# Kernel tuning notes

Hardware: AMD Instinct MI355X
Metric: run time of the kernel (lower is better)

Reference implementation:

```python
import jax, jax.numpy as jnp
import numpy as np
from jax import lax

H = 2048          # hidden_size
I = 1408          # moe_intermediate_size
E = 16            # n_routed_experts
K = 4             # num_experts_per_tok
N_SHARED = 2      # n_shared_experts
IS = I * N_SHARED # shared expert intermediate
B, S = 1, 1024


def setup_inputs() -> dict:
    key = jax.random.key(0)
    ks = jax.random.split(key, 8)
    scale = 0.02
    return {
        "hidden_states": jax.random.normal(ks[0], (B, S, H), dtype=jnp.float32),
        "gate_w": jax.random.normal(ks[1], (E, H), dtype=jnp.float32) * scale,  # MoEGate.weight
        "w_gate": jax.random.normal(ks[2], (E, H, I), dtype=jnp.float32) * scale,
        "w_up": jax.random.normal(ks[3], (E, H, I), dtype=jnp.float32) * scale,
        "w_down": jax.random.normal(ks[4], (E, I, H), dtype=jnp.float32) * scale,
        "sw_gate": jax.random.normal(ks[5], (H, IS), dtype=jnp.float32) * scale,
        "sw_up": jax.random.normal(ks[6], (H, IS), dtype=jnp.float32) * scale,
        "sw_down": jax.random.normal(ks[7], (IS, H), dtype=jnp.float32) * scale,
    }


def _moe_forward(hidden_states, gate_w, w_gate, w_up, w_down, sw_gate, sw_up, sw_down):
    bsz, seq_len, h = hidden_states.shape
    flat = hidden_states.reshape(-1, h)                # [T, H]
    T = flat.shape[0]

    # --- MoEGate: softmax scoring + top-k (norm_topk_prob=False) ---
    logits = flat @ gate_w.T                           # [T, E]
    scores = jax.nn.softmax(logits, axis=-1)
    topk_w, topk_idx = lax.top_k(scores, K)            # [T, K]

    # combine[t, e] = sum of top-k weights assigned to expert e (scatter of dispatch)
    combine = jnp.zeros((T, E), dtype=flat.dtype).at[
        jnp.arange(T)[:, None], topk_idx
    ].add(topk_w)                                      # [T, E]

    # --- routed experts: scan over experts, accumulate weighted SwiGLU MLP outputs ---
    def step(y, xs):
        wg, wu, wd, c = xs                             # [H,I], [H,I], [I,H], [T]
        out = (jax.nn.silu(flat @ wg) * (flat @ wu)) @ wd   # [T, H]
        return y + c[:, None] * out, None

    y, _ = lax.scan(step, jnp.zeros_like(flat), (w_gate, w_up, w_down, combine.T))

    # --- shared experts (always-on SwiGLU MLP with larger intermediate) ---
    shared = (jax.nn.silu(flat @ sw_gate) * (flat @ sw_up)) @ sw_down  # [T, H]

    return (y + shared).reshape(bsz, seq_len, h)


def reference(hidden_states, gate_w, w_gate, w_up, w_down, sw_gate, sw_up, sw_down):
    return _moe_forward(hidden_states, gate_w, w_gate, w_up, w_down,
                        sw_gate, sw_up, sw_down)
```

## Files before the change

### kernel.cpp

```cpp
#include <hip/hip_runtime.h>
#include <hip/hip_bf16.h>
#include <stdint.h>

#define T_TOK 1024
#define H_DIM 2048
#define I_DIM 1408
#define E_NUM 16
#define K_TOP 4
#define IS_DIM 2816
#define BK 64
#define BKP 72
#define BM 256
#define NT_MAX 40

typedef __hip_bfloat16 bf;
typedef __attribute__((ext_vector_type(8))) __bf16 bf16x8;
typedef __attribute__((ext_vector_type(4))) float f32x4;

__device__ __forceinline__ void gload16(const void* g, void* l) {
  __builtin_amdgcn_global_load_lds((const __attribute__((address_space(1))) void*)g,
                                   (__attribute__((address_space(3))) void*)l, 16, 0, 0);
}

__global__ void cvt_x_kernel(const float* __restrict__ in, bf* __restrict__ out) {
  int i = blockIdx.x * blockDim.x + threadIdx.x;
  float4 v = reinterpret_cast<const float4*>(in)[i];
  int b = i * 4;
  out[b + 0] = __float2bfloat16(v.x);
  out[b + 1] = __float2bfloat16(v.y);
  out[b + 2] = __float2bfloat16(v.z);
  out[b + 3] = __float2bfloat16(v.w);
}

__global__ void gate_topk_kernel(const float* __restrict__ x, const float* __restrict__ gw,
                                 int* __restrict__ topk_idx, float* __restrict__ topk_w) {
  int t = blockIdx.x;
  int lane = threadIdx.x;
  float acc[E_NUM];
#pragma unroll
  for (int e = 0; e < E_NUM; e++) acc[e] = 0.f;
  const float* xt = x + (long)t * H_DIM;
  for (int h = lane; h < H_DIM; h += 64) {
    float xv = xt[h];
#pragma unroll
    for (int e = 0; e < E_NUM; e++) acc[e] += xv * gw[e * H_DIM + h];
  }
#pragma unroll
  for (int e = 0; e < E_NUM; e++) {
    float v = acc[e];
    for (int off = 32; off; off >>= 1) v += __shfl_xor(v, off, 64);
    acc[e] = v;
  }
  if (lane == 0) {
    float m = acc[0];
#pragma unroll
    for (int e = 1; e < E_NUM; e++) m = fmaxf(m, acc[e]);
    float sc[E_NUM];
    float s = 0.f;
#pragma unroll
    for (int e = 0; e < E_NUM; e++) { sc[e] = expf(acc[e] - m); s += sc[e]; }
    float inv = 1.f / s;
#pragma unroll
    for (int e = 0; e < E_NUM; e++) sc[e] *= inv;
    for (int k = 0; k < K_TOP; k++) {
      int bi = 0;
      float bv = sc[0];
      for (int e = 1; e < E_NUM; e++)
        if (sc[e] > bv) { bv = sc[e]; bi = e; }
      topk_idx[t * K_TOP + k] = bi;
      topk_w[t * K_TOP + k] = bv;
      sc[bi] = -1.f;
    }
  }
}

__global__ void build_lists_kernel(const int* __restrict__ topk_idx,
                                   int* __restrict__ rows, int* __restrict__ tile_expert,
                                   int* __restrict__ n_tiles) {
  __shared__ int cnt[E_NUM], cur[E_NUM], s_tb;
  int tid = threadIdx.x;
  if (tid < E_NUM) cnt[tid] = 0;
  __syncthreads();
  for (int p = tid; p < T_TOK * K_TOP; p += blockDim.x)
    atomicAdd(&cnt[topk_idx[p]], 1);
  __syncthreads();
  if (tid == 0) {
    int tb = 0;
    for (int e = 0; e < E_NUM; e++) {
      int nt = (cnt[e] + BM - 1) / BM;
      cur[e] = tb * BM;
      for (int j = 0; j < nt; j++) tile_expert[tb + j] = e;
      tb += nt;
    }
    for (int j = 0; j < 8; j++) tile_expert[tb + j] = 16 + (j >> 2);
    s_tb = tb;
    *n_tiles = tb + 8;
  }
  __syncthreads();
  int tb = s_tb;
  for (int r = tid; r < NT_MAX * BM; r += blockDim.x) rows[r] = -1;
  __syncthreads();
  for (int p = tid; p < T_TOK * K_TOP; p += blockDim.x) {
    int t = p >> 2, k = p & 3;
    int e = topk_idx[p];
    int slot = atomicAdd(&cur[e], 1);
    rows[slot] = t * 8 + k;
  }
  for (int idx = tid; idx < 8 * BM; idx += blockDim.x) {
    int j = idx >> 8, r = idx & 255;
    int t = (j & 3) * BM + r;
    rows[(tb + j) * BM + r] = t * 8 + 4 + (j >> 2);
  }
}

__launch_bounds__(512, 4)
__global__ void gemm_gateup_kernel(const bf* __restrict__ xb,
                                   const int* __restrict__ rows,
                                   const int* __restrict__ tile_expert,
                                   const int* __restrict__ n_tiles,
                                   const float* __restrict__ Wg,
                                   const float* __restrict__ Wu,
                                   const float* __restrict__ SWg,
                                   const float* __restrict__ SWu,
                                   bf* __restrict__ act) {
  int bid = blockIdx.x;
  int idx = (bid & 7) * 110 + (bid >> 3);
  int x = idx / NT_MAX, rt = idx % NT_MAX;
  if (rt >= *n_tiles) return;
  int e = tile_expert[rt];
  bool sh = e >= 16;
  const float* gbase = sh ? (SWg + (e - 16) * I_DIM) : (Wg + (long)e * H_DIM * I_DIM);
  const float* ubase = sh ? (SWu + (e - 16) * I_DIM) : (Wu + (long)e * H_DIM * I_DIM);
  long bstride = sh ? IS_DIM : I_DIM;
  int i0 = x * 64;

  __shared__ bf lA[BM * BK];
  __shared__ bf lB2[2][64 * BKP];

  int tid = threadIdx.x, w = tid >> 6, lane = tid & 63;
  int l15 = lane & 15, lhi = lane >> 4;
  int nq = tid & 15, mt = (tid >> 4) & 1, kq = (tid >> 5) & 7, jh = tid >> 8;
  int sswz = (((lane & 7) ^ (lane >> 3)) * 8);
  int bco = (kq ^ (nq & 7)) * 8 + jh * 4;

  const bf* asrc[4];
#pragma unroll
  for (int i = 0; i < 4; i++) {
    int rr = rt * BM + i * 64 + w * 8 + (lane >> 3);
    int p = rows[rr];
    int tok = (p >= 0) ? (p >> 3) : 0;
    asrc[i] = xb + (long)tok * H_DIM + sswz;
  }

  const float* psrc = (mt ? ubase : gbase) + i0 + nq * 4 + (long)(kq * 8 + jh * 4) * bstride;

  f32x4 accg[4][2], accu[4][2];
  f32x4 z4 = {0.f, 0.f, 0.f, 0.f};
#pragma unroll
  for (int m = 0; m < 4; m++)
#pragma unroll
    for (int n = 0; n < 2; n++) { accg[m][n] = z4; accu[m][n] = z4; }

  int wr = w >> 1, wc = w & 1;
  for (int kt = 0; kt < H_DIM; kt += BK) {
    float4 v[4];
    const float* p_ = psrc + (long)kt * bstride;
#pragma unroll
    for (int j = 0; j < 4; j++)
      v[j] = *reinterpret_cast<const float4*>(p_ + (long)j * bstride);
    __syncthreads();
#pragma unroll
    for (int i = 0; i < 4; i++)
      gload16(asrc[i] + kt, lA + (i * 64 + w * 8) * BK);
#pragma unroll
    for (int c = 0; c < 4; c++) {
      union { short4 s4; bf b[4]; } o;
#pragma unroll
      for (int j = 0; j < 4; j++)
        o.b[j] = __float2bfloat16(((const float*)&v[j])[c]);
      *reinterpret_cast<short4*>(&lB2[mt][(nq * 4 + c) * BKP + bco]) = o.s4;
    }
    __syncthreads();
#pragma unroll
    for (int kk = 0; kk < 2; kk++) {
      bf16x8 af[4];
#pragma unroll
      for (int m = 0; m < 4; m++)
        af[m] = *reinterpret_cast<const bf16x8*>(
            lA + (wr * 64 + m * 16 + l15) * BK + (((kk * 4 + lhi) ^ (l15 & 7)) * 8));
#pragma unroll
      for (int n = 0; n < 2; n++) {
        int nrow = wc * 32 + n * 16 + l15;
        int bch = ((kk * 4 + lhi) ^ ((nrow >> 2) & 7)) * 8;
        bf16x8 gf = *reinterpret_cast<const bf16x8*>(&lB2[0][nrow * BKP + bch]);
        bf16x8 uf = *reinterpret_cast<const bf16x8*>(&lB2[1][nrow * BKP + bch]);
#pragma unroll
        for (int m = 0; m < 4; m++) {
          accg[m][n] = __builtin_amdgcn_mfma_f32_16x16x32_bf16(af[m], gf, accg[m][n], 0, 0, 0);
          accu[m][n] = __builtin_amdgcn_mfma_f32_16x16x32_bf16(af[m], uf, accu[m][n], 0, 0, 0);
        }
      }
    }
  }

#pragma unroll
  for (int m = 0; m < 4; m++)
#pragma unroll
    for (int n = 0; n < 2; n++)
#pragma unroll
      for (int r2 = 0; r2 < 4; r2++) {
        float gv = accg[m][n][r2];
        float uv = accu[m][n][r2];
        float s = (gv / (1.f + __expf(-gv))) * uv;
        int row = rt * BM + wr * 64 + m * 16 + lhi * 4 + r2;
        int col = i0 + wc * 32 + n * 16 + l15;
        act[(long)row * I_DIM + col] = __float2bfloat16(s);
      }
}

__launch_bounds__(512, 4)
__global__ void gemm_down_kernel(const bf* __restrict__ A,
                                 const int* __restrict__ rows,
                                 const int* __restrict__ tile_expert,
                                 const int* __restrict__ n_tiles,
                                 const float* __restrict__ Wd,
                                 const float* __restrict__ SWd,
                                 bf* __restrict__ outp) {
  int bid = blockIdx.x;
  int idx = (bid & 7) * 80 + (bid >> 3);
  int x = idx / NT_MAX, rt = idx % NT_MAX;
  if (rt >= *n_tiles) return;
  int e = tile_expert[rt];
  bool sh = e >= 16;
  const float* bbase = sh ? (SWd + (long)(e - 16) * I_DIM * H_DIM)
                          : (Wd + (long)e * I_DIM * H_DIM);
  int h0 = x * 128;

  __shared__ bf lA[BM * BK];
  __shared__ bf lB[128 * BKP];
  __shared__ int rowsl[BM];

  int tid = threadIdx.x, w = tid >> 6, lane = tid & 63;
  int l15 = lane & 15, lhi = lane >> 4;
  int ng = tid & 31, kq = (tid >> 5) & 7, jh = tid >> 8;
  int sswz = (((lane & 7) ^ (lane >> 3)) * 8);
  int bco = (kq ^ (ng & 7)) * 8 + jh * 4;
  if (tid < BM) rowsl[tid] = rows[rt * BM + tid];

  const bf* asrc[4];
#pragma unroll
  for (int i = 0; i < 4; i++)
    asrc[i] = A + (long)(rt * BM + i * 64 + w * 8 + (lane >> 3)) * I_DIM + sswz;

  const float* psrc = bbase + h0 + ng * 4 + (long)(kq * 8 + jh * 4) * H_DIM;

  f32x4 acc[4][4];
  f32x4 z4 = {0.f, 0.f, 0.f, 0.f};
#pragma unroll
  for (int m = 0; m < 4; m++)
#pragma unroll
    for (int n = 0; n < 4; n++) acc[m][n] = z4;

  int wr = w >> 1, wc = w & 1;
  for (int kt = 0; kt < I_DIM; kt += BK) {
    float4 v[4];
    const float* p_ = psrc + (long)kt * H_DIM;
#pragma unroll
    for (int j = 0; j < 4; j++)
      v[j] = *reinterpret_cast<const float4*>(p_ + (long)j * H_DIM);
    __syncthreads();
#pragma unroll
    for (int i = 0; i < 4; i++)
      gload16(asrc[i] + kt, lA + (i * 64 + w * 8) * BK);
#pragma unroll
    for (int c = 0; c < 4; c++) {
      union { short4 s4; bf b[4]; } o;
#pragma unroll
      for (int j = 0; j < 4; j++)
        o.b[j] = __float2bfloat16(((const float*)&v[j])[c]);
      *reinterpret_cast<short4*>(&lB[(ng * 4 + c) * BKP + bco]) = o.s4;
    }
    __syncthreads();
#pragma unroll
    for (int kk = 0; kk < 2; kk++) {
      bf16x8 af[4];
#pragma unroll
      for (int m = 0; m < 4; m++)
        af[m] = *reinterpret_cast<const bf16x8*>(
            lA + (wr * 64 + m * 16 + l15) * BK + (((kk * 4 + lhi) ^ (l15 & 7)) * 8));
#pragma unroll
      for (int n = 0; n < 4; n++) {
        int nrow = wc * 64 + n * 16 + l15;
        int bch = ((kk * 4 + lhi) ^ ((nrow >> 2) & 7)) * 8;
        bf16x8 bfr = *reinterpret_cast<const bf16x8*>(&lB[nrow * BKP + bch]);
#pragma unroll
        for (int m = 0; m < 4; m++)
          acc[m][n] = __builtin_amdgcn_mfma_f32_16x16x32_bf16(af[m], bfr, acc[m][n], 0, 0, 0);
      }
    }
  }

#pragma unroll
  for (int m = 0; m < 4; m++)
#pragma unroll
    for (int n = 0; n < 4; n++)
#pragma unroll
      for (int r2 = 0; r2 < 4; r2++) {
        int lrow = wr * 64 + m * 16 + lhi * 4 + r2;
        int col = h0 + wc * 64 + n * 16 + l15;
        int p = rowsl[lrow];
        if (p >= 0) outp[(long)p * H_DIM + col] = __float2bfloat16(acc[m][n][r2]);
      }
}

__global__ void combine_kernel(const bf* __restrict__ outp,
                               const float* __restrict__ topk_w,
                               float* __restrict__ out) {
  int g = blockIdx.x * blockDim.x + threadIdx.x;
  int t = g >> 8;
  int h = (g & 255) * 8;
  const bf* base = outp + (long)t * 8 * H_DIM + h;
  float w0 = topk_w[t * 4 + 0], w1 = topk_w[t * 4 + 1];
  float w2 = topk_w[t * 4 + 2], w3 = topk_w[t * 4 + 3];
  bf16x8 s4 = *reinterpret_cast<const bf16x8*>(base + 4 * H_DIM);
  bf16x8 s5 = *reinterpret_cast<const bf16x8*>(base + 5 * H_DIM);
  bf16x8 r0 = *reinterpret_cast<const bf16x8*>(base + 0 * H_DIM);
  bf16x8 r1 = *reinterpret_cast<const bf16x8*>(base + 1 * H_DIM);
  bf16x8 r2 = *reinterpret_cast<const bf16x8*>(base + 2 * H_DIM);
  bf16x8 r3 = *reinterpret_cast<const bf16x8*>(base + 3 * H_DIM);
  float acc[8];
#pragma unroll
  for (int j = 0; j < 8; j++) {
    acc[j] = (float)s4[j] + (float)s5[j]
           + w0 * (float)r0[j] + w1 * (float)r1[j]
           + w2 * (float)r2[j] + w3 * (float)r3[j];
  }
  float4* o = reinterpret_cast<float4*>(out + (long)t * H_DIM + h);
  o[0] = make_float4(acc[0], acc[1], acc[2], acc[3]);
  o[1] = make_float4(acc[4], acc[5], acc[6], acc[7]);
}

extern "C" void kernel_launch(void* const* d_in, const int* in_sizes, int n_in,
                              void* d_out, int out_size, void* d_ws, size_t ws_size,
                              hipStream_t stream) {
  const float* x     = (const float*)d_in[0];
  const float* gw    = (const float*)d_in[1];
  const float* wgate = (const float*)d_in[2];
  const float* wup   = (const float*)d_in[3];
  const float* wdown = (const float*)d_in[4];
  const float* swg   = (const float*)d_in[5];
  const float* swu   = (const float*)d_in[6];
  const float* swd   = (const float*)d_in[7];
  float* out = (float*)d_out;

  char* ws = (char*)d_ws;
  size_t off = 0;
  auto alloc = [&](size_t bytes) {
    void* p = ws + off;
    off += (bytes + 255) & ~(size_t)255;
    return p;
  };

  bf* xb   = (bf*)alloc((size_t)T_TOK * H_DIM * 2);
  bf* act  = (bf*)alloc((size_t)NT_MAX * BM * I_DIM * 2);
  bf* outp = (bf*)alloc((size_t)T_TOK * 8 * H_DIM * 2);
  int*   topk_idx = (int*)alloc(T_TOK * K_TOP * 4);
  float* topk_w   = (float*)alloc(T_TOK * K_TOP * 4);
  int*   rowsbuf  = (int*)alloc(NT_MAX * BM * 4);
  int*   tile_exp = (int*)alloc(NT_MAX * 4);
  int*   n_tiles  = (int*)alloc(64);
  (void)ws_size; (void)in_sizes; (void)n_in; (void)out_size;

  hipLaunchKernelGGL(cvt_x_kernel, dim3(T_TOK * H_DIM / 1024), dim3(256), 0, stream, x, xb);
  hipLaunchKernelGGL(gate_topk_kernel, dim3(T_TOK), dim3(64), 0, stream, x, gw, topk_idx, topk_w);
  hipLaunchKernelGGL(build_lists_kernel, dim3(1), dim3(256), 0, stream, topk_idx, rowsbuf, tile_exp, n_tiles);

  hipLaunchKernelGGL(gemm_gateup_kernel, dim3(22 * NT_MAX), dim3(512), 0, stream,
                     xb, rowsbuf, tile_exp, n_tiles, wgate, wup, swg, swu, act);
  hipLaunchKernelGGL(gemm_down_kernel, dim3(16 * NT_MAX), dim3(512), 0, stream,
                     act, rowsbuf, tile_exp, n_tiles, wdown, swd, outp);

  hipLaunchKernelGGL(combine_kernel, dim3(T_TOK * H_DIM / 8 / 256), dim3(256), 0, stream,
                     outp, topk_w, out);
}
```

Before: 321.9 us.

## Double-buffer GEMM K-loop with async fp32 weight staging through LDS

New measurement: 472.9 us. 1.47x slower.

```diff
diff --git a/kernel.cpp b/kernel.cpp
--- a/kernel.cpp
+++ b/kernel.cpp
@@ -113,7 +113,7 @@
   }
 }
 
-__launch_bounds__(512, 4)
+__launch_bounds__(512, 2)
 __global__ void gemm_gateup_kernel(const bf* __restrict__ xb,
                                    const int* __restrict__ rows,
                                    const int* __restrict__ tile_expert,
@@ -134,14 +134,13 @@
   long bstride = sh ? IS_DIM : I_DIM;
   int i0 = x * 64;
 
-  __shared__ bf lA[BM * BK];
+  __shared__ bf lA[2][BM * BK];
+  __shared__ float stg[2][2][64 * 64];
   __shared__ bf lB2[2][64 * BKP];
 
   int tid = threadIdx.x, w = tid >> 6, lane = tid & 63;
   int l15 = lane & 15, lhi = lane >> 4;
-  int nq = tid & 15, mt = (tid >> 4) & 1, kq = (tid >> 5) & 7, jh = tid >> 8;
   int sswz = (((lane & 7) ^ (lane >> 3)) * 8);
-  int bco = (kq ^ (nq & 7)) * 8 + jh * 4;
 
   const bf* asrc[4];
 #pragma unroll
@@ -152,7 +151,12 @@
     asrc[i] = xb + (long)tok * H_DIM + sswz;
   }
 
-  const float* psrc = (mt ? ubase : gbase) + i0 + nq * 4 + (long)(kq * 8 + jh * 4) * bstride;
+  int bwm = w >> 2;
+  const float* bmat = bwm ? ubase : gbase;
+  const float* bsrc = bmat + i0 + (lane & 15) * 4 + (long)((w & 3) * 16 + (lane >> 4)) * bstride;
+  int brow = (w & 3) * 16;
+
+  int cnq = tid & 15, ckh = (tid >> 4) & 1, ckg = (tid >> 5) & 7, cmt = tid >> 8;
 
   f32x4 accg[4][2], accu[4][2];
   f32x4 z4 = {0.f, 0.f, 0.f, 0.f};
@@ -162,46 +166,69 @@
     for (int n = 0; n < 2; n++) { accg[m][n] = z4; accu[m][n] = z4; }
 
   int wr = w >> 1, wc = w & 1;
-  for (int kt = 0; kt < H_DIM; kt += BK) {
-    float4 v[4];
-    const float* p_ = psrc + (long)kt * bstride;
-#pragma unroll
-    for (int j = 0; j < 4; j++)
-      v[j] = *reinterpret_cast<const float4*>(p_ + (long)j * bstride);
-    __syncthreads();
-#pragma unroll
-    for (int i = 0; i < 4; i++)
-      gload16(asrc[i] + kt, lA + (i * 64 + w * 8) * BK);
-#pragma unroll
-    for (int c = 0; c < 4; c++) {
-      union { short4 s4; bf b[4]; } o;
-#pragma unroll
-      for (int j = 0; j < 4; j++)
-        o.b[j] = __float2bfloat16(((const float*)&v[j])[c]);
-      *reinterpret_cast<short4*>(&lB2[mt][(nq * 4 + c) * BKP + bco]) = o.s4;
-    }
-    __syncthreads();
-#pragma unroll
-    for (int kk = 0; kk < 2; kk++) {
-      bf16x8 af[4];
-#pragma unroll
-      for (int m = 0; m < 4; m++)
-        af[m] = *reinterpret_cast<const bf16x8*>(
-            lA + (wr * 64 + m * 16 + l15) * BK + (((kk * 4 + lhi) ^ (l15 & 7)) * 8));
-#pragma unroll
-      for (int n = 0; n < 2; n++) {
-        int nrow = wc * 32 + n * 16 + l15;
-        int bch = ((kk * 4 + lhi) ^ ((nrow >> 2) & 7)) * 8;
-        bf16x8 gf = *reinterpret_cast<const bf16x8*>(&lB2[0][nrow * BKP + bch]);
-        bf16x8 uf = *reinterpret_cast<const bf16x8*>(&lB2[1][nrow * BKP + bch]);
-#pragma unroll
-        for (int m = 0; m < 4; m++) {
-          accg[m][n] = __builtin_amdgcn_mfma_f32_16x16x32_bf16(af[m], gf, accg[m][n], 0, 0, 0);
-          accu[m][n] = __builtin_amdgcn_mfma_f32_16x16x32_bf16(af[m], uf, accu[m][n], 0, 0, 0);
-        }
-      }
-    }
-  }
+
+#define GU_ISSUE(T, NB)                                                              \
+  {                                                                                  \
+    _Pragma("unroll") for (int i = 0; i < 4; i++)                                    \
+        gload16(asrc[i] + (T) * BK, &lA[NB][(i * 64 + w * 8) * BK]);                 \
+    const float* bs_ = bsrc + (long)(T) * BK * bstride;                              \
+    _Pragma("unroll") for (int q = 0; q < 4; q++)                                    \
+        gload16(bs_ + (long)(q * 4) * bstride, &stg[NB][bwm][(brow + q * 4) * 64]);  \
+  }
+
+#define GU_CONVERT(CB)                                                               \
+  {                                                                                  \
+    float4 cv[4];                                                                    \
+    _Pragma("unroll") for (int j = 0; j < 4; j++)                                    \
+        cv[j] = *reinterpret_cast<const float4*>(                                    \
+            &stg[CB][cmt][(ckg * 8 + ckh * 4 + j) * 64 + cnq * 4]);                  \
+    _Pragma("unroll") for (int c = 0; c < 4; c++) {                                  \
+      union { short4 s4; bf b[4]; } o;                                               \
+      _Pragma("unroll") for (int j = 0; j < 4; j++)                                  \
+          o.b[j] = __float2bfloat16(((const float*)&cv[j])[c]);                      \
+      *reinterpret_cast<short4*>(                                                    \
+          &lB2[cmt][(cnq * 4 + c) * BKP + (ckg ^ (cnq & 7)) * 8 + ckh * 4]) = o.s4;  \
+    }                                                                                \
+  }
+
+#define GU_MFMA(CB)                                                                  \
+  {                                                                                  \
+    _Pragma("unroll") for (int kk = 0; kk < 2; kk++) {                               \
+      bf16x8 af[4];                                                                  \
+      _Pragma("unroll") for (int m = 0; m < 4; m++)                                  \
+          af[m] = *reinterpret_cast<const bf16x8*>(                                  \
+              &lA[CB][(wr * 64 + m * 16 + l15) * BK + (((kk * 4 + lhi) ^ (l15 & 7)) * 8)]); \
+      _Pragma("unroll") for (int n = 0; n < 2; n++) {                                \
+        int nrow = wc * 32 + n * 16 + l15;                                           \
+        int bch = ((kk * 4 + lhi) ^ ((nrow >> 2) & 7)) * 8;                          \
+        bf16x8 gf = *reinterpret_cast<const bf16x8*>(&lB2[0][nrow * BKP + bch]);     \
+        bf16x8 uf = *reinterpret_cast<const bf16x8*>(&lB2[1][nrow * BKP + bch]);     \
+        _Pragma("unroll") for (int m = 0; m < 4; m++) {                              \
+          accg[m][n] = __builtin_amdgcn_mfma_f32_16x16x32_bf16(af[m], gf, accg[m][n], 0, 0, 0); \
+          accu[m][n] = __builtin_amdgcn_mfma_f32_16x16x32_bf16(af[m], uf, accu[m][n], 0, 0, 0); \
+        }                                                                            \
+      }                                                                              \
+    }                                                                                \
+  }
+
+  const int NT = H_DIM / BK;
+  GU_ISSUE(0, 0);
+
+  for (int t = 0; t < NT; ++t) {
+    int cur = t & 1, nxt = cur ^ 1;
+    asm volatile("s_waitcnt vmcnt(0)" ::: "memory");
+    __builtin_amdgcn_s_barrier();
+    __builtin_amdgcn_sched_barrier(0);
+    if (t + 1 < NT) GU_ISSUE(t + 1, nxt);
+    GU_CONVERT(cur);
+    asm volatile("s_waitcnt lgkmcnt(0)" ::: "memory");
+    __builtin_amdgcn_s_barrier();
+    __builtin_amdgcn_sched_barrier(0);
+    GU_MFMA(cur);
+  }
+#undef GU_ISSUE
+#undef GU_CONVERT
+#undef GU_MFMA
 
 #pragma unroll
   for (int m = 0; m < 4; m++)
@@ -218,7 +245,7 @@
       }
 }
 
-__launch_bounds__(512, 4)
+__launch_bounds__(512, 2)
 __global__ void gemm_down_kernel(const bf* __restrict__ A,
                                  const int* __restrict__ rows,
                                  const int* __restrict__ tile_expert,
@@ -236,15 +263,14 @@
                           : (Wd + (long)e * I_DIM * H_DIM);
   int h0 = x * 128;
 
-  __shared__ bf lA[BM * BK];
+  __shared__ bf lA[2][BM * BK];
+  __shared__ float stg[2][64 * 128];
   __shared__ bf lB[128 * BKP];
   __shared__ int rowsl[BM];
 
   int tid = threadIdx.x, w = tid >> 6, lane = tid & 63;
   int l15 = lane & 15, lhi = lane >> 4;
-  int ng = tid & 31, kq = (tid >> 5) & 7, jh = tid >> 8;
   int sswz = (((lane & 7) ^ (lane >> 3)) * 8);
-  int bco = (kq ^ (ng & 7)) * 8 + jh * 4;
   if (tid < BM) rowsl[tid] = rows[rt * BM + tid];
 
   const bf* asrc[4];
@@ -252,7 +278,10 @@
   for (int i = 0; i < 4; i++)
     asrc[i] = A + (long)(rt * BM + i * 64 + w * 8 + (lane >> 3)) * I_DIM + sswz;
 
-  const float* psrc = bbase + h0 + ng * 4 + (long)(kq * 8 + jh * 4) * H_DIM;
+  const float* bsrc = bbase + h0 + (lane & 31) * 4 + (long)(w * 8 + (lane >> 5)) * H_DIM;
+  int brow = w * 8;
+
+  int cng = tid & 31, ckg = (tid >> 5) & 7, cch = tid >> 8;
 
   f32x4 acc[4][4];
   f32x4 z4 = {0.f, 0.f, 0.f, 0.f};
@@ -262,43 +291,66 @@
     for (int n = 0; n < 4; n++) acc[m][n] = z4;
 
   int wr = w >> 1, wc = w & 1;
-  for (int kt = 0; kt < I_DIM; kt += BK) {
-    float4 v[4];
-    const float* p_ = psrc + (long)kt * H_DIM;
-#pragma unroll
-    for (int j = 0; j < 4; j++)
-      v[j] = *reinterpret_cast<const float4*>(p_ + (long)j * H_DIM);
-    __syncthreads();
-#pragma unroll
-    for (int i = 0; i < 4; i++)
-      gload16(asrc[i] + kt, lA + (i * 64 + w * 8) * BK);
-#pragma unroll
-    for (int c = 0; c < 4; c++) {
-      union { short4 s4; bf b[4]; } o;
-#pragma unroll
-      for (int j = 0; j < 4; j++)
-        o.b[j] = __float2bfloat16(((const float*)&v[j])[c]);
-      *reinterpret_cast<short4*>(&lB[(ng * 4 + c) * BKP + bco]) = o.s4;
-    }
-    __syncthreads();
-#pragma unroll
-    for (int kk = 0; kk < 2; kk++) {
-      bf16x8 af[4];
-#pragma unroll
-      for (int m = 0; m < 4; m++)
-        af[m] = *reinterpret_cast<const bf16x8*>(
-            lA + (wr * 64 + m * 16 + l15) * BK + (((kk * 4 + lhi) ^ (l15 & 7)) * 8));
-#pragma unroll
-      for (int n = 0; n < 4; n++) {
-        int nrow = wc * 64 + n * 16 + l15;
-        int bch = ((kk * 4 + lhi) ^ ((nrow >> 2) & 7)) * 8;
-        bf16x8 bfr = *reinterpret_cast<const bf16x8*>(&lB[nrow * BKP + bch]);
-#pragma unroll
-        for (int m = 0; m < 4; m++)
-          acc[m][n] = __builtin_amdgcn_mfma_f32_16x16x32_bf16(af[m], bfr, acc[m][n], 0, 0, 0);
-      }
-    }
-  }
+
+#define DN_ISSUE(T, NB)                                                              \
+  {                                                                                  \
+    _Pragma("unroll") for (int i = 0; i < 4; i++)                                    \
+        gload16(asrc[i] + (T) * BK, &lA[NB][(i * 64 + w * 8) * BK]);                 \
+    const float* bs_ = bsrc + (long)(T) * BK * H_DIM;                                \
+    _Pragma("unroll") for (int q = 0; q < 4; q++)                                    \
+        gload16(bs_ + (long)(q * 2) * H_DIM, &stg[NB][(brow + q * 2) * 128]);        \
+  }
+
+#define DN_CONVERT(CB)                                                              \
+  {                                                                                 \
+    float2 cv[8];                                                                   \
+    _Pragma("unroll") for (int j = 0; j < 8; j++)                                   \
+        cv[j] = *reinterpret_cast<const float2*>(                                   \
+            &stg[CB][(ckg * 8 + j) * 128 + cng * 4 + cch * 2]);                     \
+    _Pragma("unroll") for (int c = 0; c < 2; c++) {                                 \
+      union { bf16x8 vv; bf b[8]; } o;                                              \
+      _Pragma("unroll") for (int j = 0; j < 8; j++)                                 \
+          o.b[j] = __float2bfloat16(((const float*)&cv[j])[c]);                     \
+      *reinterpret_cast<bf16x8*>(                                                   \
+          &lB[(cng * 4 + cch * 2 + c) * BKP + (ckg ^ (cng & 7)) * 8]) = o.vv;       \
+    }                                                                               \
+  }
+
+#define DN_MFMA(CB)                                                                 \
+  {                                                                                 \
+    _Pragma("unroll") for (int kk = 0; kk < 2; kk++) {                              \
+      bf16x8 af[4];                                                                 \
+      _Pragma("unroll") for (int m = 0; m < 4; m++)                                 \
+          af[m] = *reinterpret_cast<const bf16x8*>(                                 \
+              &lA[CB][(wr * 64 + m * 16 + l15) * BK + (((kk * 4 + lhi) ^ (l15 & 7)) * 8)]); \
+      _Pragma("unroll") for (int n = 0; n < 4; n++) {                               \
+        int nrow = wc * 64 + n * 16 + l15;                                          \
+        int bch = ((kk * 4 + lhi) ^ ((nrow >> 2) & 7)) * 8;                         \
+        bf16x8 bfr = *reinterpret_cast<const bf16x8*>(&lB[nrow * BKP + bch]);       \
+        _Pragma("unroll") for (int m = 0; m < 4; m++)                               \
+            acc[m][n] = __builtin_amdgcn_mfma_f32_16x16x32_bf16(af[m], bfr, acc[m][n], 0, 0, 0); \
+      }                                                                             \
+    }                                                                               \
+  }
+
+  const int NT = I_DIM / BK;
+  DN_ISSUE(0, 0);
+
+  for (int t = 0; t < NT; ++t) {
+    int cur = t & 1, nxt = cur ^ 1;
+    asm volatile("s_waitcnt vmcnt(0)" ::: "memory");
+    __builtin_amdgcn_s_barrier();
+    __builtin_amdgcn_sched_barrier(0);
+    if (t + 1 < NT) DN_ISSUE(t + 1, nxt);
+    DN_CONVERT(cur);
+    asm volatile("s_waitcnt lgkmcnt(0)" ::: "memory");
+    __builtin_amdgcn_s_barrier();
+    __builtin_amdgcn_sched_barrier(0);
+    DN_MFMA(cur);
+  }
+#undef DN_ISSUE
+#undef DN_CONVERT
+#undef DN_MFMA
 
 #pragma unroll
   for (int m = 0; m < 4; m++)
```

## Retile MoE GEMMs to 384-row tiles with narrower N and 6 waves

Applied to the files above, without the earlier changes.

After: 459.7 us. +42.8%, slower.

```diff
diff --git a/kernel.cpp b/kernel.cpp
--- a/kernel.cpp
+++ b/kernel.cpp
@@ -10,8 +10,8 @@
 #define IS_DIM 2816
 #define BK 64
 #define BKP 72
-#define BM 256
-#define NT_MAX 40
+#define BM 384
+#define NT_MAX 32
 
 typedef __hip_bfloat16 bf;
 typedef __attribute__((ext_vector_type(8))) __bf16 bf16x8;
@@ -92,9 +92,9 @@
       for (int j = 0; j < nt; j++) tile_expert[tb + j] = e;
       tb += nt;
     }
-    for (int j = 0; j < 8; j++) tile_expert[tb + j] = 16 + (j >> 2);
+    for (int j = 0; j < 6; j++) tile_expert[tb + j] = 16 + (j / 3);
     s_tb = tb;
-    *n_tiles = tb + 8;
+    *n_tiles = tb + 6;
   }
   __syncthreads();
   int tb = s_tb;
@@ -106,14 +106,14 @@
     int slot = atomicAdd(&cur[e], 1);
     rows[slot] = t * 8 + k;
   }
-  for (int idx = tid; idx < 8 * BM; idx += blockDim.x) {
-    int j = idx >> 8, r = idx & 255;
-    int t = (j & 3) * BM + r;
-    rows[(tb + j) * BM + r] = t * 8 + 4 + (j >> 2);
-  }
-}
-
-__launch_bounds__(512, 4)
+  for (int idx = tid; idx < 6 * BM; idx += blockDim.x) {
+    int j = idx / BM, r = idx % BM;
+    int t = (j % 3) * BM + r;
+    if (t < T_TOK) rows[(tb + j) * BM + r] = t * 8 + 4 + (j / 3);
+  }
+}
+
+__launch_bounds__(384, 2)
 __global__ void gemm_gateup_kernel(const bf* __restrict__ xb,
                                    const int* __restrict__ rows,
                                    const int* __restrict__ tile_expert,
@@ -124,36 +124,37 @@
                                    const float* __restrict__ SWu,
                                    bf* __restrict__ act) {
   int bid = blockIdx.x;
-  int idx = (bid & 7) * 110 + (bid >> 3);
-  int x = idx / NT_MAX, rt = idx % NT_MAX;
+  int idx = (bid & 7) * 176 + (bid >> 3);
+  int x = idx >> 5, rt = idx & 31;
   if (rt >= *n_tiles) return;
   int e = tile_expert[rt];
   bool sh = e >= 16;
   const float* gbase = sh ? (SWg + (e - 16) * I_DIM) : (Wg + (long)e * H_DIM * I_DIM);
   const float* ubase = sh ? (SWu + (e - 16) * I_DIM) : (Wu + (long)e * H_DIM * I_DIM);
   long bstride = sh ? IS_DIM : I_DIM;
-  int i0 = x * 64;
+  int i0 = x * 32;
 
   __shared__ bf lA[BM * BK];
-  __shared__ bf lB2[2][64 * BKP];
+  __shared__ bf lB2[2][32 * BKP];
 
   int tid = threadIdx.x, w = tid >> 6, lane = tid & 63;
   int l15 = lane & 15, lhi = lane >> 4;
-  int nq = tid & 15, mt = (tid >> 4) & 1, kq = (tid >> 5) & 7, jh = tid >> 8;
   int sswz = (((lane & 7) ^ (lane >> 3)) * 8);
-  int bco = (kq ^ (nq & 7)) * 8 + jh * 4;
-
-  const bf* asrc[4];
-#pragma unroll
-  for (int i = 0; i < 4; i++) {
-    int rr = rt * BM + i * 64 + w * 8 + (lane >> 3);
+
+  bool stager = tid < 256;
+  int smat = tid >> 7, sr = tid & 127, nc = sr & 7, kq = sr >> 3;
+  const float* psrc = (smat ? ubase : gbase) + i0 + nc * 4 + (long)(kq * 4) * bstride;
+  int bslot = (((kq >> 1) ^ nc) * 16 + (kq & 1) * 8) / 2;
+
+  const bf* asrc[8];
+#pragma unroll
+  for (int i = 0; i < 8; i++) {
+    int rr = rt * BM + i * 48 + w * 8 + (lane >> 3);
     int p = rows[rr];
     int tok = (p >= 0) ? (p >> 3) : 0;
     asrc[i] = xb + (long)tok * H_DIM + sswz;
   }
 
-  const float* psrc = (mt ? ubase : gbase) + i0 + nq * 4 + (long)(kq * 8 + jh * 4) * bstride;
-
   f32x4 accg[4][2], accu[4][2];
   f32x4 z4 = {0.f, 0.f, 0.f, 0.f};
 #pragma unroll
@@ -161,24 +162,27 @@
 #pragma unroll
     for (int n = 0; n < 2; n++) { accg[m][n] = z4; accu[m][n] = z4; }
 
-  int wr = w >> 1, wc = w & 1;
   for (int kt = 0; kt < H_DIM; kt += BK) {
     float4 v[4];
-    const float* p_ = psrc + (long)kt * bstride;
-#pragma unroll
-    for (int j = 0; j < 4; j++)
-      v[j] = *reinterpret_cast<const float4*>(p_ + (long)j * bstride);
+    if (stager) {
+      const float* p_ = psrc + (long)kt * bstride;
+#pragma unroll
+      for (int j = 0; j < 4; j++)
+        v[j] = *reinterpret_cast<const float4*>(p_ + (long)j * bstride);
+    }
     __syncthreads();
 #pragma unroll
-    for (int i = 0; i < 4; i++)
-      gload16(asrc[i] + kt, lA + (i * 64 + w * 8) * BK);
-#pragma unroll
-    for (int c = 0; c < 4; c++) {
-      union { short4 s4; bf b[4]; } o;
-#pragma unroll
-      for (int j = 0; j < 4; j++)
-        o.b[j] = __float2bfloat16(((const float*)&v[j])[c]);
-      *reinterpret_cast<short4*>(&lB2[mt][(nq * 4 + c) * BKP + bco]) = o.s4;
+    for (int i = 0; i < 8; i++)
+      gload16(asrc[i] + kt, lA + (i * 48 + w * 8) * BK);
+    if (stager) {
+#pragma unroll
+      for (int c = 0; c < 4; c++) {
+        union { short4 s4; bf b[4]; } o;
+#pragma unroll
+        for (int j = 0; j < 4; j++)
+          o.b[j] = __float2bfloat16(((const float*)&v[j])[c]);
+        *reinterpret_cast<short4*>(&lB2[smat][(nc * 4 + c) * BKP + bslot]) = o.s4;
+      }
     }
     __syncthreads();
 #pragma unroll
@@ -187,10 +191,10 @@
 #pragma unroll
       for (int m = 0; m < 4; m++)
         af[m] = *reinterpret_cast<const bf16x8*>(
-            lA + (wr * 64 + m * 16 + l15) * BK + (((kk * 4 + lhi) ^ (l15 & 7)) * 8));
+            lA + (w * 64 + m * 16 + l15) * BK + (((kk * 4 + lhi) ^ (l15 & 7)) * 8));
 #pragma unroll
       for (int n = 0; n < 2; n++) {
-        int nrow = wc * 32 + n * 16 + l15;
+        int nrow = n * 16 + l15;
         int bch = ((kk * 4 + lhi) ^ ((nrow >> 2) & 7)) * 8;
         bf16x8 gf = *reinterpret_cast<const bf16x8*>(&lB2[0][nrow * BKP + bch]);
         bf16x8 uf = *reinterpret_cast<const bf16x8*>(&lB2[1][nrow * BKP + bch]);
@@ -212,13 +216,13 @@
         float gv = accg[m][n][r2];
         float uv = accu[m][n][r2];
         float s = (gv / (1.f + __expf(-gv))) * uv;
-        int row = rt * BM + wr * 64 + m * 16 + lhi * 4 + r2;
-        int col = i0 + wc * 32 + n * 16 + l15;
+        int row = rt * BM + w * 64 + m * 16 + lhi * 4 + r2;
+        int col = i0 + n * 16 + l15;
         act[(long)row * I_DIM + col] = __float2bfloat16(s);
       }
 }
 
-__launch_bounds__(512, 4)
+__launch_bounds__(384, 2)
 __global__ void gemm_down_kernel(const bf* __restrict__ A,
                                  const int* __restrict__ rows,
                                  const int* __restrict__ tile_expert,
@@ -227,32 +231,33 @@
                                  const float* __restrict__ SWd,
                                  bf* __restrict__ outp) {
   int bid = blockIdx.x;
-  int idx = (bid & 7) * 80 + (bid >> 3);
-  int x = idx / NT_MAX, rt = idx % NT_MAX;
+  int idx = (bid & 7) * 128 + (bid >> 3);
+  int x = idx >> 5, rt = idx & 31;
   if (rt >= *n_tiles) return;
   int e = tile_expert[rt];
   bool sh = e >= 16;
   const float* bbase = sh ? (SWd + (long)(e - 16) * I_DIM * H_DIM)
                           : (Wd + (long)e * I_DIM * H_DIM);
-  int h0 = x * 128;
+  int h0 = x * 64;
 
   __shared__ bf lA[BM * BK];
-  __shared__ bf lB[128 * BKP];
+  __shared__ bf lB[64 * BKP];
   __shared__ int rowsl[BM];
 
   int tid = threadIdx.x, w = tid >> 6, lane = tid & 63;
   int l15 = lane & 15, lhi = lane >> 4;
-  int ng = tid & 31, kq = (tid >> 5) & 7, jh = tid >> 8;
   int sswz = (((lane & 7) ^ (lane >> 3)) * 8);
-  int bco = (kq ^ (ng & 7)) * 8 + jh * 4;
-  if (tid < BM) rowsl[tid] = rows[rt * BM + tid];
-
-  const bf* asrc[4];
-#pragma unroll
-  for (int i = 0; i < 4; i++)
-    asrc[i] = A + (long)(rt * BM + i * 64 + w * 8 + (lane >> 3)) * I_DIM + sswz;
-
-  const float* psrc = bbase + h0 + ng * 4 + (long)(kq * 8 + jh * 4) * H_DIM;
+  for (int r = tid; r < BM; r += 384) rowsl[r] = rows[rt * BM + r];
+
+  bool stager = tid < 256;
+  int nc = tid & 15, kq = tid >> 4;
+  const float* psrc = bbase + h0 + nc * 4 + (long)(kq * 4) * H_DIM;
+  int bslot = (((kq >> 1) ^ (nc & 7)) * 16 + (kq & 1) * 8) / 2;
+
+  const bf* asrc[8];
+#pragma unroll
+  for (int i = 0; i < 8; i++)
+    asrc[i] = A + (long)(rt * BM + i * 48 + w * 8 + (lane >> 3)) * I_DIM + sswz;
 
   f32x4 acc[4][4];
   f32x4 z4 = {0.f, 0.f, 0.f, 0.f};
@@ -261,24 +266,27 @@
 #pragma unroll
     for (int n = 0; n < 4; n++) acc[m][n] = z4;
 
-  int wr = w >> 1, wc = w & 1;
   for (int kt = 0; kt < I_DIM; kt += BK) {
     float4 v[4];
-    const float* p_ = psrc + (long)kt * H_DIM;
-#pragma unroll
-    for (int j = 0; j < 4; j++)
-      v[j] = *reinterpret_cast<const float4*>(p_ + (long)j * H_DIM);
+    if (stager) {
+      const float* p_ = psrc + (long)kt * H_DIM;
+#pragma unroll
+      for (int j = 0; j < 4; j++)
+        v[j] = *reinterpret_cast<const float4*>(p_ + (long)j * H_DIM);
+    }
     __syncthreads();
 #pragma unroll
-    for (int i = 0; i < 4; i++)
-      gload16(asrc[i] + kt, lA + (i * 64 + w * 8) * BK);
-#pragma unroll
-    for (int c = 0; c < 4; c++) {
-      union { short4 s4; bf b[4]; } o;
-#pragma unroll
-      for (int j = 0; j < 4; j++)
-        o.b[j] = __float2bfloat16(((const float*)&v[j])[c]);
-      *reinterpret_cast<short4*>(&lB[(ng * 4 + c) * BKP + bco]) = o.s4;
+    for (int i = 0; i < 8; i++)
+      gload16(asrc[i] + kt, lA + (i * 48 + w * 8) * BK);
+    if (stager) {
+#pragma unroll
+      for (int c = 0; c < 4; c++) {
+        union { short4 s4; bf b[4]; } o;
+#pragma unroll
+        for (int j = 0; j < 4; j++)
+          o.b[j] = __float2bfloat16(((const float*)&v[j])[c]);
+        *reinterpret_cast<short4*>(&lB[(nc * 4 + c) * BKP + bslot]) = o.s4;
+      }
     }
     __syncthreads();
 #pragma unroll
@@ -287,10 +295,10 @@
 #pragma unroll
       for (int m = 0; m < 4; m++)
         af[m] = *reinterpret_cast<const bf16x8*>(
-            lA + (wr * 64 + m * 16 + l15) * BK + (((kk * 4 + lhi) ^ (l15 & 7)) * 8));
+            lA + (w * 64 + m * 16 + l15) * BK + (((kk * 4 + lhi) ^ (l15 & 7)) * 8));
 #pragma unroll
       for (int n = 0; n < 4; n++) {
-        int nrow = wc * 64 + n * 16 + l15;
+        int nrow = n * 16 + l15;
         int bch = ((kk * 4 + lhi) ^ ((nrow >> 2) & 7)) * 8;
         bf16x8 bfr = *reinterpret_cast<const bf16x8*>(&lB[nrow * BKP + bch]);
 #pragma unroll
@@ -306,8 +314,8 @@
     for (int n = 0; n < 4; n++)
 #pragma unroll
       for (int r2 = 0; r2 < 4; r2++) {
-        int lrow = wr * 64 + m * 16 + lhi * 4 + r2;
-        int col = h0 + wc * 64 + n * 16 + l15;
+        int lrow = w * 64 + m * 16 + lhi * 4 + r2;
+        int col = h0 + n * 16 + l15;
         int p = rowsl[lrow];
         if (p >= 0) outp[(long)p * H_DIM + col] = __float2bfloat16(acc[m][n][r2]);
       }
@@ -375,9 +383,9 @@
   hipLaunchKernelGGL(gate_topk_kernel, dim3(T_TOK), dim3(64), 0, stream, x, gw, topk_idx, topk_w);
   hipLaunchKernelGGL(build_lists_kernel, dim3(1), dim3(256), 0, stream, topk_idx, rowsbuf, tile_exp, n_tiles);
 
-  hipLaunchKernelGGL(gemm_gateup_kernel, dim3(22 * NT_MAX), dim3(512), 0, stream,
+  hipLaunchKernelGGL(gemm_gateup_kernel, dim3((I_DIM / 32) * NT_MAX), dim3(384), 0, stream,
                      xb, rowsbuf, tile_exp, n_tiles, wgate, wup, swg, swu, act);
-  hipLaunchKernelGGL(gemm_down_kernel, dim3(16 * NT_MAX), dim3(512), 0, stream,
+  hipLaunchKernelGGL(gemm_down_kernel, dim3((H_DIM / 64) * NT_MAX), dim3(384), 0, stream,
                      act, rowsbuf, tile_exp, n_tiles, wdown, swd, outp);
 
   hipLaunchKernelGGL(combine_kernel, dim3(T_TOK * H_DIM / 8 / 256), dim3(256), 0, stream,
```
